# Optimization experiments

Hardware: AMD Instinct MI355X
Metric: run time of the kernel (lower is better)

## Reference

```python
import jax, jax.numpy as jnp
import numpy as np

T, B, K, N, M = 1024, 32, 8, 64, 64
DELTA = 3  # number of passes: DELTA-1 states-only + 1 final with output


def setup_inputs():
    key = jax.random.key(0)
    ks = jax.random.split(key, 7)
    x = jax.random.normal(ks[0], (T, B, K), jnp.float32)
    # stable, a.s.-distinct complex eigenvalues: |lam| in [0.5, 0.99)
    mag = jax.random.uniform(ks[1], (K, N), jnp.float32, 0.5, 0.99)
    phase = jax.random.uniform(ks[2], (K, N), jnp.float32, -np.pi, np.pi)
    lam_re = mag * jnp.cos(phase)
    lam_im = mag * jnp.sin(phase)
    C_re = jax.random.normal(ks[3], (K, N, M), jnp.float32) / np.sqrt(N)
    C_im = jax.random.normal(ks[4], (K, N, M), jnp.float32) / np.sqrt(N)
    D = jax.random.normal(ks[5], (K, M), jnp.float32)
    Do = jax.random.normal(ks[6], (K, M), jnp.float32)
    return {"x": x, "lam_re": lam_re, "lam_im": lam_im,
            "C_re": C_re, "C_im": C_im, "D": D, "Do": Do}


def _compute_Bp(lam):
    # Bʹ[k,j] = exp(-sum_i log(1 - lam_i/lam_j)), diagonal ratio zeroed
    k, n = lam.shape
    ratios = lam[:, :, None] / lam[:, None, :]           # (k, n, n)
    eye = jnp.eye(n, dtype=bool)[None]
    ratios = jnp.where(eye, jnp.zeros((), ratios.dtype), ratios)
    lnBp = -jnp.sum(jnp.log(1.0 - ratios), axis=1)       # (k, n)
    return jnp.exp(lnBp)


def _linear_recurrence(a, bx):
    # s_t = a_t * s_{t-1} + bx_t, computed as a parallel associative scan
    def comb(l, r):
        al, bl = l
        ar, br = r
        return (al * ar, bl * ar + br)
    _, s = jax.lax.associative_scan(comb, (a, bx), axis=0)
    return s


def _states(xc, lam, Bp, alpha):
    # one pass of the complex diagonal SSM; returns states (T, B, K, N)
    Bpx = (xc[..., None] * Bp).reshape(T, B, K * N)       # Bʹ·x
    if alpha is None:
        al = jnp.broadcast_to(lam.reshape(1, 1, K * N), (T, B, K * N))
    else:
        al = (alpha * lam[None, None]).reshape(T, B, K * N)  # α·λ
    # standard=True: shift inputs by one step (prepend zeros, drop last)
    z = jnp.zeros((1, B, K * N), al.dtype)
    al = jnp.concatenate([z, al[:-1]], axis=0)
    Bpx = jnp.concatenate([z, Bpx[:-1]], axis=0)
    return _linear_recurrence(al, Bpx).reshape(T, B, K, N)


def _forward(x, lam_re, lam_im, C_re, C_im, D, Do):
    lam = (lam_re + 1j * lam_im).astype(jnp.complex64)    # (K, N)
    Cp = (C_re + 1j * C_im).astype(jnp.complex64)         # (K, N, M)
    xc = x.astype(jnp.complex64)                          # (T, B, K)
    Bp = _compute_Bp(lam)                                 # (K, N)

    alpha = None
    for _ in range(DELTA - 1):
        s = _states(xc, lam, Bp, alpha)                   # (T, B, K, N)
        ls = lam[None, None] * s                          # λ·sʹ
        alpha = 1.0 / jnp.sqrt(1.0 + ls * jnp.conj(ls))   # recipsq

    s = _states(xc, lam, Bp, alpha)                       # final pass
    Cs = jnp.einsum("tbkn,knm->tbkm", s, Cp)              # Cʹ·sʹ
    Dx = xc[..., None] * D.astype(jnp.complex64)          # D·x
    y = Cs + Dx + Do.astype(jnp.complex64)                # (T, B, K, M)
    return jnp.mean(y, axis=2)                            # average over k


def reference(x, lam_re, lam_im, C_re, C_im, D, Do):
    return _forward(x, lam_re, lam_im, C_re, C_im, D, Do)
```

## Files before the change

### kernel.cpp

```cpp
#include <hip/hip_runtime.h>

#define TT 1024
#define BB 32
#define KKD 8
#define NN 64
#define MM 64
#define BKC (BB*KKD)
#define KN  (KKD*NN)
#define SS 16
#define LL 64

typedef __attribute__((ext_vector_type(8))) _Float16 f16x8;
typedef __attribute__((ext_vector_type(2))) __fp16 fp16x2;
typedef __attribute__((ext_vector_type(4))) float f32x4;

#define SC_DOWN (1.0f/4096.0f)
#define SC_UP   512.0f


static __device__ __forceinline__ float bcast(float v, int lane) {
    return __builtin_bit_cast(float,
        __builtin_amdgcn_readlane(__builtin_bit_cast(int, v), lane));
}

__global__ __launch_bounds__(64) void bp_kernel(const float* __restrict__ lam_re,
                                                const float* __restrict__ lam_im,
                                                float* __restrict__ bp) {
    int k = blockIdx.x;
    int j = threadIdx.x;
    double ljre = (double)lam_re[k*NN+j], ljim = (double)lam_im[k*NN+j];
    double dj = ljre*ljre + ljim*ljim;
    double pre = 1.0, pim = 0.0;
    for (int i = 0; i < NN; ++i) {
        if (i == j) continue;
        double lire = (double)lam_re[k*NN+i], liim = (double)lam_im[k*NN+i];
        double rre = (lire*ljre + liim*ljim)/dj;
        double rim = (liim*ljre - lire*ljim)/dj;
        double zre = 1.0 - rre, zim = -rim;
        double zd = zre*zre + zim*zim;
        double npre = (pre*zre + pim*zim)/zd;
        double npim = (pim*zre - pre*zim)/zd;
        pre = npre; pim = npim;
    }
    bp[(k*NN+j)*2+0] = (float)pre;
    bp[(k*NN+j)*2+1] = (float)pim;
}

__global__ __launch_bounds__(256) void wprep_kernel(const float* __restrict__ C_re,
                                                    const float* __restrict__ C_im,
                                                    unsigned short* __restrict__ Wt) {
    int idx = blockIdx.x*256 + threadIdx.x;
    int m  = idx >> 10;
    int j  = idx & 1023;
    int kn = j >> 1;
    float v = (j & 1) ? -C_im[kn*MM + m] : C_re[kn*MM + m];
    Wt[idx] = __builtin_bit_cast(unsigned short, (_Float16)(v * SC_UP));
}

__global__ __launch_bounds__(1024, 4) void scan_par_kernel(const float* __restrict__ x,
                                                           const float* __restrict__ lam_re,
                                                           const float* __restrict__ lam_im,
                                                           const float* __restrict__ bp,
                                                           unsigned int* __restrict__ abuf,
                                                           int TL) {
    __shared__ float e1[SS][64][2];
    __shared__ float e2[SS][64][2];
    __shared__ float e3[SS][64][2];
    __shared__ float pa2[SS][64];
    __shared__ float pa3[SS][64];

    int bk = blockIdx.x;
    int b = bk >> 3;
    int k = bk & 7;
    int tid = threadIdx.x;
    int q = tid >> 6;
    int n = tid & 63;
    int kn = k*NN + n;
    float lre = lam_re[kn], lim = lam_im[kn];
    float bpre = bp[2*kn+0], bpim = bp[2*kn+1];
    float l2 = lre*lre + lim*lim;

    float p64re = lre, p64im = lim;
    #pragma unroll
    for (int i = 0; i < 6; ++i) {
        float tr = p64re*p64re - p64im*p64im;
        float ti = 2.f*p64re*p64im;
        p64re = tr; p64im = ti;
    }

    const float* xp = x + (size_t)(q*LL)*BKC + b*KKD + k;
    float xs = xp[(size_t)n * BKC];

    float s1re = 0.f, s1im = 0.f;
    #pragma unroll 16
    for (int i = 0; i < LL; ++i) {
        float xv = bcast(xs, i);
        float ure = xv*bpre, uim = xv*bpim;
        float tre = __builtin_fmaf(lre, s1re, __builtin_fmaf(-lim, s1im, ure));
        float tim = __builtin_fmaf(lre, s1im, __builtin_fmaf( lim, s1re, uim));
        s1re = tre; s1im = tim;
    }
    e1[q][n][0] = s1re; e1[q][n][1] = s1im;
    __syncthreads();
    float c1re = 0.f, c1im = 0.f;
    for (int i = 0; i < q; ++i) {
        float tre = __builtin_fmaf(p64re, c1re, __builtin_fmaf(-p64im, c1im, e1[i][n][0]));
        float tim = __builtin_fmaf(p64re, c1im, __builtin_fmaf( p64im, c1re, e1[i][n][1]));
        c1re = tre; c1im = tim;
    }

    s1re = c1re; s1im = c1im;
    float s2re = 0.f, s2im = 0.f, pa = 1.f;
    #pragma unroll 16
    for (int i = 0; i < LL; ++i) {
        float xv = bcast(xs, i);
        float ure = xv*bpre, uim = xv*bpim;
        float mm1 = __builtin_fmaf(l2, __builtin_fmaf(s1re, s1re, s1im*s1im), 1.f);
        float a1 = rsqrtf(mm1);
        float t1re = __builtin_fmaf(lre, s1re, __builtin_fmaf(-lim, s1im, ure));
        float t1im = __builtin_fmaf(lre, s1im, __builtin_fmaf( lim, s1re, uim));
        s1re = t1re; s1im = t1im;
        float cr = a1*lre, ci = a1*lim;
        float t2re = __builtin_fmaf(cr, s2re, __builtin_fmaf(-ci, s2im, ure));
        float t2im = __builtin_fmaf(cr, s2im, __builtin_fmaf( ci, s2re, uim));
        s2re = t2re; s2im = t2im;
        pa *= a1;
    }
    e2[q][n][0] = s2re; e2[q][n][1] = s2im; pa2[q][n] = pa;
    __syncthreads();
    float c2re = 0.f, c2im = 0.f;
    for (int i = 0; i < q; ++i) {
        float pai = pa2[i][n];
        float qre = pai*p64re, qim = pai*p64im;
        float tre = __builtin_fmaf(qre, c2re, __builtin_fmaf(-qim, c2im, e2[i][n][0]));
        float tim = __builtin_fmaf(qre, c2im, __builtin_fmaf( qim, c2re, e2[i][n][1]));
        c2re = tre; c2im = tim;
    }

    s1re = c1re; s1im = c1im;
    s2re = c2re; s2im = c2im;
    float s3re = 0.f, s3im = 0.f, pb = 1.f;
    unsigned int a2pk[LL/2];
    float a2prev = 0.f;
    #pragma unroll
    for (int i = 0; i < LL; ++i) {
        float xv = bcast(xs, i);
        float ure = xv*bpre, uim = xv*bpim;
        float mm1 = __builtin_fmaf(l2, __builtin_fmaf(s1re, s1re, s1im*s1im), 1.f);
        float a1 = rsqrtf(mm1);
        float t1re = __builtin_fmaf(lre, s1re, __builtin_fmaf(-lim, s1im, ure));
        float t1im = __builtin_fmaf(lre, s1im, __builtin_fmaf( lim, s1re, uim));
        s1re = t1re; s1im = t1im;
        float mm2 = __builtin_fmaf(l2, __builtin_fmaf(s2re, s2re, s2im*s2im), 1.f);
        float a2 = rsqrtf(mm2);
        float cr = a1*lre, ci = a1*lim;
        float t2re = __builtin_fmaf(cr, s2re, __builtin_fmaf(-ci, s2im, ure));
        float t2im = __builtin_fmaf(cr, s2im, __builtin_fmaf( ci, s2re, uim));
        s2re = t2re; s2im = t2im;
        float dr = a2*lre, di = a2*lim;
        float t3re = __builtin_fmaf(dr, s3re, __builtin_fmaf(-di, s3im, ure));
        float t3im = __builtin_fmaf(dr, s3im, __builtin_fmaf( di, s3re, uim));
        s3re = t3re; s3im = t3im;
        pb *= a2;
        if (i & 1)
            a2pk[i>>1] = __builtin_bit_cast(unsigned int,
                           __builtin_amdgcn_cvt_pkrtz(a2prev, a2));
        else
            a2prev = a2;
    }
    e3[q][n][0] = s3re; e3[q][n][1] = s3im; pa3[q][n] = pb;
    __syncthreads();
    float c3re = 0.f, c3im = 0.f;
    for (int i = 0; i < q; ++i) {
        float pbi = pa3[i][n];
        float qre = pbi*p64re, qim = pbi*p64im;
        float tre = __builtin_fmaf(qre, c3re, __builtin_fmaf(-qim, c3im, e3[i][n][0]));
        float tim = __builtin_fmaf(qre, c3im, __builtin_fmaf( qim, c3re, e3[i][n][1]));
        c3re = tre; c3im = tim;
    }

    s3re = c3re; s3im = c3im;
    unsigned int* ap = abuf + (size_t)bk*TL*64 + (size_t)(q*LL)*64 + n;
    #pragma unroll
    for (int i = 0; i < LL; ++i) {
        fp16x2 hv = __builtin_amdgcn_cvt_pkrtz(s3re*SC_DOWN, s3im*SC_DOWN);
        ap[(size_t)i * 64] = __builtin_bit_cast(unsigned int, hv);
        float xv = bcast(xs, i);
        float ure = xv*bpre, uim = xv*bpim;
        unsigned int pk = a2pk[i>>1];
        unsigned short h = (i & 1) ? (unsigned short)(pk >> 16)
                                   : (unsigned short)(pk & 0xffffu);
        float a2 = (float)__builtin_bit_cast(_Float16, h);
        float dr = a2*lre, di = a2*lim;
        float t3re = __builtin_fmaf(dr, s3re, __builtin_fmaf(-di, s3im, ure));
        float t3im = __builtin_fmaf(dr, s3im, __builtin_fmaf( di, s3re, uim));
        s3re = t3re; s3im = t3im;
    }
}

__global__ __launch_bounds__(64) void scan_seq_kernel(const float* __restrict__ x,
                                                      const float* __restrict__ lam_re,
                                                      const float* __restrict__ lam_im,
                                                      const float* __restrict__ bp,
                                                      float* __restrict__ state,
                                                      unsigned int* __restrict__ abuf,
                                                      int chunk_start, int chunk_len,
                                                      int TL) {
    int bk = blockIdx.x;
    int b = bk >> 3;
    int k = bk & 7;
    int n = threadIdx.x;
    int kn = k*NN + n;
    float lre = lam_re[kn], lim = lam_im[kn];
    float bpre = bp[2*kn+0], bpim = bp[2*kn+1];
    float l2 = lre*lre + lim*lim;
    int chain = bk*NN + n;

    float s1re,s1im,s2re,s2im,s3re,s3im;
    if (chunk_start == 0) {
        s1re=s1im=s2re=s2im=s3re=s3im=0.f;
    } else {
        const float* st = state + (size_t)chain*6;
        s1re=st[0];s1im=st[1];s2re=st[2];s2im=st[3];s3re=st[4];s3im=st[5];
    }

    const float* xp = x + (size_t)chunk_start*BKC + b*KKD + k;
    unsigned int* ap = abuf + (size_t)bk*TL*64 + n;

    float xs = xp[(size_t)n * BKC];
    for (int t0 = 0; t0 < chunk_len; t0 += 64) {
        float xs_nxt = 0.f;
        if (t0 + 64 < chunk_len) xs_nxt = xp[(size_t)(t0 + 64 + n) * BKC];
        #pragma unroll
        for (int w = 0; w < 4; ++w) {
            float mm_[16], cre[16], cim[16];
            #pragma unroll
            for (int j = 0; j < 16; ++j) {
                float xv = bcast(xs, w*16 + j);
                mm_[j] = __builtin_fmaf(l2, s1re*s1re + s1im*s1im, 1.0f);
                float ure = xv*bpre, uim = xv*bpim;
                float tre = __builtin_fmaf(lre, s1re, __builtin_fmaf(-lim, s1im, ure));
                float tim = __builtin_fmaf(lre, s1im, __builtin_fmaf( lim, s1re, uim));
                s1re=tre; s1im=tim;
            }
            #pragma unroll
            for (int j = 0; j < 16; ++j) {
                float a = rsqrtf(mm_[j]); cre[j] = a*lre; cim[j] = a*lim;
            }
            #pragma unroll
            for (int j = 0; j < 16; ++j) {
                float xv = bcast(xs, w*16 + j);
                mm_[j] = __builtin_fmaf(l2, s2re*s2re + s2im*s2im, 1.0f);
                float ure = xv*bpre, uim = xv*bpim;
                float tre = __builtin_fmaf(cre[j], s2re, __builtin_fmaf(-cim[j], s2im, ure));
                float tim = __builtin_fmaf(cre[j], s2im, __builtin_fmaf( cim[j], s2re, uim));
                s2re=tre; s2im=tim;
            }
            #pragma unroll
            for (int j = 0; j < 16; ++j) {
                float a = rsqrtf(mm_[j]); cre[j] = a*lre; cim[j] = a*lim;
            }
            #pragma unroll
            for (int j = 0; j < 16; ++j) {
                fp16x2 hv = __builtin_amdgcn_cvt_pkrtz(s3re*SC_DOWN, s3im*SC_DOWN);
                ap[(size_t)(t0 + w*16 + j) * 64] = __builtin_bit_cast(unsigned int, hv);
                float xv = bcast(xs, w*16 + j);
                float ure = xv*bpre, uim = xv*bpim;
                float tre = __builtin_fmaf(cre[j], s3re, __builtin_fmaf(-cim[j], s3im, ure));
                float tim = __builtin_fmaf(cre[j], s3im, __builtin_fmaf( cim[j], s3re, uim));
                s3re=tre; s3im=tim;
            }
        }
        xs = xs_nxt;
    }
    float* st = state + (size_t)chain*6;
    st[0]=s1re;st[1]=s1im;st[2]=s2re;st[3]=s2im;st[4]=s3re;st[5]=s3im;
}

__global__ __launch_bounds__(256) void proj_kernel(const unsigned int* __restrict__ A,
                                                   const unsigned short* __restrict__ Wt,
                                                   const float* __restrict__ x,
                                                   const float* __restrict__ D,
                                                   const float* __restrict__ Do,
                                                   float* __restrict__ out,
                                                   int rowOff, int TL) {
    __shared__ uint4 At[2][1024];
    __shared__ uint4 Wb[2][1024];
    int tid = threadIdx.x;
    int w = tid >> 6, l = tid & 63;
    int lg = l >> 4, lr = l & 15;
    int wr = w >> 1, wc = w & 1;
    int bI = blockIdx.x;
    int R0 = bI * 64;

    f32x4 acc[2][2];
    #pragma unroll
    for (int g = 0; g < 2; ++g)
        #pragma unroll
        for (int t = 0; t < 2; ++t) acc[g][t] = (f32x4){0.f,0.f,0.f,0.f};

    uint4 ra[4], rw[4];
    int srow[4], su[4];
    #pragma unroll
    for (int i = 0; i < 4; ++i) {
        int unit = w*256 + i*64 + l;
        srow[i] = unit >> 4;
        su[i]   = unit & 15;
    }

    #pragma unroll
    for (int i = 0; i < 4; ++i) {
        int row = srow[i], u = su[i];
        int b = row & 31, t2 = (bI << 1) + (row >> 5);
        ra[i] = *(const uint4*)((const char*)A + ((((size_t)(b*8 + 0)*TL + t2) << 8) + u*16));
        rw[i] = *(const uint4*)((const char*)Wt + (row*2048 + 0*256 + u*16));
    }
    #pragma unroll
    for (int i = 0; i < 4; ++i) {
        int row = srow[i], u = su[i];
        At[0][row*16 + (u ^ (row & 7))] = ra[i];
        Wb[0][row*16 + (u ^ (row & 7))] = rw[i];
    }
    __syncthreads();

    for (int kc = 0; kc < 8; ++kc) {
        int cur = kc & 1;
        if (kc < 7) {
            int kn = kc + 1;
            #pragma unroll
            for (int i = 0; i < 4; ++i) {
                int row = srow[i], u = su[i];
                int b = row & 31, t2 = (bI << 1) + (row >> 5);
                ra[i] = *(const uint4*)((const char*)A + ((((size_t)(b*8 + kn)*TL + t2) << 8) + u*16));
                rw[i] = *(const uint4*)((const char*)Wt + (row*2048 + kn*256 + u*16));
            }
        }
        #pragma unroll
        for (int ks = 0; ks < 4; ++ks) {
            f16x8 af[2], bf[2];
            #pragma unroll
            for (int g = 0; g < 2; ++g) {
                int row = (wr*2 + g)*16 + lr;
                af[g] = __builtin_bit_cast(f16x8, At[cur][row*16 + ((ks*4 + lg) ^ (row & 7))]);
            }
            #pragma unroll
            for (int t = 0; t < 2; ++t) {
                int m = (wc*2 + t)*16 + lr;
                bf[t] = __builtin_bit_cast(f16x8, Wb[cur][m*16 + ((ks*4 + lg) ^ (m & 7))]);
            }
            #pragma unroll
            for (int g = 0; g < 2; ++g)
                #pragma unroll
                for (int t = 0; t < 2; ++t)
                    acc[g][t] = __builtin_amdgcn_mfma_f32_16x16x32_f16(af[g], bf[t], acc[g][t], 0,0,0);
        }
        if (kc < 7) {
            int nb = (kc + 1) & 1;
            #pragma unroll
            for (int i = 0; i < 4; ++i) {
                int row = srow[i], u = su[i];
                At[nb][row*16 + (u ^ (row & 7))] = ra[i];
                Wb[nb][row*16 + (u ^ (row & 7))] = rw[i];
            }
        }
        __syncthreads();
    }

    #pragma unroll
    for (int g = 0; g < 2; ++g) {
        int rowA = rowOff + R0 + (wr*2 + g)*16 + lr;
        const float* xr = x + (size_t)rowA * KKD;
        float4 x0 = *(const float4*)(xr);
        float4 x1 = *(const float4*)(xr + 4);
        f16x8 a2;
        a2[0] = (lg==0) ? (_Float16)x0.x : ((lg==1) ? (_Float16)1.0f : (_Float16)0.0f);
        a2[1] = (lg==0) ? (_Float16)x0.y : (_Float16)0.0f;
        a2[2] = (lg==0) ? (_Float16)x0.z : (_Float16)0.0f;
        a2[3] = (lg==0) ? (_Float16)x0.w : (_Float16)0.0f;
        a2[4] = (lg==0) ? (_Float16)x1.x : (_Float16)0.0f;
        a2[5] = (lg==0) ? (_Float16)x1.y : (_Float16)0.0f;
        a2[6] = (lg==0) ? (_Float16)x1.z : (_Float16)0.0f;
        a2[7] = (lg==0) ? (_Float16)x1.w : (_Float16)0.0f;
        #pragma unroll
        for (int t = 0; t < 2; ++t) {
            int c = (wc*2 + t)*16 + lr;
            float dob = 0.f;
            #pragma unroll
            for (int i = 0; i < 8; ++i) dob += Do[i*64 + c];
            f16x8 b2;
            b2[0] = (lg==0) ? (_Float16)(D[0*64+c]*0.125f)
                  : ((lg==1) ? (_Float16)(dob*0.125f) : (_Float16)0.0f);
            b2[1] = (lg==0) ? (_Float16)(D[1*64+c]*0.125f) : (_Float16)0.0f;
            b2[2] = (lg==0) ? (_Float16)(D[2*64+c]*0.125f) : (_Float16)0.0f;
            b2[3] = (lg==0) ? (_Float16)(D[3*64+c]*0.125f) : (_Float16)0.0f;
            b2[4] = (lg==0) ? (_Float16)(D[4*64+c]*0.125f) : (_Float16)0.0f;
            b2[5] = (lg==0) ? (_Float16)(D[5*64+c]*0.125f) : (_Float16)0.0f;
            b2[6] = (lg==0) ? (_Float16)(D[6*64+c]*0.125f) : (_Float16)0.0f;
            b2[7] = (lg==0) ? (_Float16)(D[7*64+c]*0.125f) : (_Float16)0.0f;
            acc[g][t] = __builtin_amdgcn_mfma_f32_16x16x32_f16(a2, b2, acc[g][t], 0,0,0);
        }
    }

    #pragma unroll
    for (int g = 0; g < 2; ++g)
        #pragma unroll
        for (int t = 0; t < 2; ++t) {
            int c = (wc*2 + t)*16 + lr;
            #pragma unroll
            for (int reg = 0; reg < 4; ++reg) {
                int row = rowOff + R0 + (wr*2 + g)*16 + lg*4 + reg;
                out[(size_t)row*MM + c] = acc[g][t][reg];
            }
        }
}

extern "C" void kernel_launch(void* const* d_in, const int* in_sizes, int n_in,
                              void* d_out, int out_size, void* d_ws, size_t ws_size,
                              hipStream_t stream) {
    const float* x      = (const float*)d_in[0];
    const float* lam_re = (const float*)d_in[1];
    const float* lam_im = (const float*)d_in[2];
    const float* C_re   = (const float*)d_in[3];
    const float* C_im   = (const float*)d_in[4];
    const float* D      = (const float*)d_in[5];
    const float* Do     = (const float*)d_in[6];
    float* out = (float*)d_out;

    char* ws = (char*)d_ws;
    float*          bpw    = (float*)(ws);
    unsigned short* Wt     = (unsigned short*)(ws + 4096);
    float*          statew = (float*)(ws + 135168);
    unsigned int*   abuf   = (unsigned int*)(ws + 528384);

    bp_kernel<<<KKD, NN, 0, stream>>>(lam_re, lam_im, bpw);
    wprep_kernel<<<256, 256, 0, stream>>>(C_re, C_im, Wt);

    const size_t base = 528384;
    const size_t perT = (size_t)BB*KN*4;

    if (ws_size >= base + (size_t)TT*perT) {
        scan_par_kernel<<<BKC, SS*64, 0, stream>>>(x, lam_re, lam_im, bpw, abuf, TT);
        proj_kernel<<<TT*BB/64, 256, 0, stream>>>(abuf, Wt, x, D, Do, out, 0, TT);
    } else {
        size_t avail = ws_size > base ? ws_size - base : 0;
        int chunkT = (int)(avail / perT) & ~63;
        if (chunkT < 64) chunkT = 64;
        for (int cs = 0; cs < TT; cs += chunkT) {
            int len = (chunkT < TT - cs) ? chunkT : (TT - cs);
            scan_seq_kernel<<<BKC, NN, 0, stream>>>(x, lam_re, lam_im, bpw, statew,
                                                    abuf, cs, len, len);
            proj_kernel<<<len*BB/64, 256, 0, stream>>>(abuf, Wt, x, D, Do, out,
                                                       cs*BB, len);
        }
    }
}
```

Measured before the change: 81.11 us.

## Split scan into 32 segments of 32 steps with half-N per block

The chunked parallel scan now splits each (b,k) problem across two blocks, each handling 32 of the 64 state channels. Each block uses 32 time segments of 32 steps instead of 16 segments of 64, which doubles the grid and halves the serial per-thread recurrence length. The cost is a longer serial carry-combine loop across segments, and x values are now shared with width-32 shuffles instead of readlane. Launch bounds request higher occupancy.

```diff
diff --git a/kernel.cpp b/kernel.cpp
--- a/kernel.cpp
+++ b/kernel.cpp
@@ -7,8 +7,6 @@
 #define MM 64
 #define BKC (BB*KKD)
 #define KN  (KKD*NN)
-#define SS 16
-#define LL 64
 
 typedef __attribute__((ext_vector_type(8))) _Float16 f16x8;
 typedef __attribute__((ext_vector_type(2))) __fp16 fp16x2;
@@ -57,63 +55,68 @@
     Wt[idx] = __builtin_bit_cast(unsigned short, (_Float16)(v * SC_UP));
 }
 
-__global__ __launch_bounds__(1024, 4) void scan_par_kernel(const float* __restrict__ x,
-                                                           const float* __restrict__ lam_re,
-                                                           const float* __restrict__ lam_im,
-                                                           const float* __restrict__ bp,
-                                                           unsigned int* __restrict__ abuf,
-                                                           int TL) {
-    __shared__ float e1[SS][64][2];
-    __shared__ float e2[SS][64][2];
-    __shared__ float e3[SS][64][2];
-    __shared__ float pa2[SS][64];
-    __shared__ float pa3[SS][64];
-
-    int bk = blockIdx.x;
+__global__ __launch_bounds__(1024, 8) void scan_par2_kernel(const float* __restrict__ x,
+                                                            const float* __restrict__ lam_re,
+                                                            const float* __restrict__ lam_im,
+                                                            const float* __restrict__ bp,
+                                                            unsigned int* __restrict__ abuf,
+                                                            int TL) {
+    __shared__ float e1[32][32][2];
+    __shared__ float e2[32][32][2];
+    __shared__ float e3[32][32][2];
+    __shared__ float pa2[32][32];
+    __shared__ float pa3[32][32];
+
+    int blk = blockIdx.x;
+    int bk = blk >> 1;
+    int h  = blk & 1;
     int b = bk >> 3;
     int k = bk & 7;
     int tid = threadIdx.x;
-    int q = tid >> 6;
-    int n = tid & 63;
-    int kn = k*NN + n;
+    int seg = tid >> 5;
+    int nl  = tid & 31;
+    int n   = h*32 + nl;
+    int kn  = k*NN + n;
+    int w    = tid >> 6;
+    int lane = tid & 63;
+
     float lre = lam_re[kn], lim = lam_im[kn];
     float bpre = bp[2*kn+0], bpim = bp[2*kn+1];
     float l2 = lre*lre + lim*lim;
 
-    float p64re = lre, p64im = lim;
-    #pragma unroll
-    for (int i = 0; i < 6; ++i) {
-        float tr = p64re*p64re - p64im*p64im;
-        float ti = 2.f*p64re*p64im;
-        p64re = tr; p64im = ti;
-    }
-
-    const float* xp = x + (size_t)(q*LL)*BKC + b*KKD + k;
-    float xs = xp[(size_t)n * BKC];
+    float p32re = lre, p32im = lim;
+    #pragma unroll
+    for (int i = 0; i < 5; ++i) {
+        float tr = p32re*p32re - p32im*p32im;
+        float ti = 2.f*p32re*p32im;
+        p32re = tr; p32im = ti;
+    }
+
+    float xs = x[(size_t)(w*64 + lane)*BKC + b*KKD + k];
 
     float s1re = 0.f, s1im = 0.f;
-    #pragma unroll 16
-    for (int i = 0; i < LL; ++i) {
-        float xv = bcast(xs, i);
+    #pragma unroll
+    for (int i = 0; i < 32; ++i) {
+        float xv = __shfl(xs, i, 32);
         float ure = xv*bpre, uim = xv*bpim;
         float tre = __builtin_fmaf(lre, s1re, __builtin_fmaf(-lim, s1im, ure));
         float tim = __builtin_fmaf(lre, s1im, __builtin_fmaf( lim, s1re, uim));
         s1re = tre; s1im = tim;
     }
-    e1[q][n][0] = s1re; e1[q][n][1] = s1im;
+    e1[seg][nl][0] = s1re; e1[seg][nl][1] = s1im;
     __syncthreads();
     float c1re = 0.f, c1im = 0.f;
-    for (int i = 0; i < q; ++i) {
-        float tre = __builtin_fmaf(p64re, c1re, __builtin_fmaf(-p64im, c1im, e1[i][n][0]));
-        float tim = __builtin_fmaf(p64re, c1im, __builtin_fmaf( p64im, c1re, e1[i][n][1]));
+    for (int i = 0; i < seg; ++i) {
+        float tre = __builtin_fmaf(p32re, c1re, __builtin_fmaf(-p32im, c1im, e1[i][nl][0]));
+        float tim = __builtin_fmaf(p32re, c1im, __builtin_fmaf( p32im, c1re, e1[i][nl][1]));
         c1re = tre; c1im = tim;
     }
 
     s1re = c1re; s1im = c1im;
     float s2re = 0.f, s2im = 0.f, pa = 1.f;
-    #pragma unroll 16
-    for (int i = 0; i < LL; ++i) {
-        float xv = bcast(xs, i);
+    #pragma unroll
+    for (int i = 0; i < 32; ++i) {
+        float xv = __shfl(xs, i, 32);
         float ure = xv*bpre, uim = xv*bpim;
         float mm1 = __builtin_fmaf(l2, __builtin_fmaf(s1re, s1re, s1im*s1im), 1.f);
         float a1 = rsqrtf(mm1);
@@ -126,25 +129,25 @@
         s2re = t2re; s2im = t2im;
         pa *= a1;
     }
-    e2[q][n][0] = s2re; e2[q][n][1] = s2im; pa2[q][n] = pa;
+    e2[seg][nl][0] = s2re; e2[seg][nl][1] = s2im; pa2[seg][nl] = pa;
     __syncthreads();
     float c2re = 0.f, c2im = 0.f;
-    for (int i = 0; i < q; ++i) {
-        float pai = pa2[i][n];
-        float qre = pai*p64re, qim = pai*p64im;
-        float tre = __builtin_fmaf(qre, c2re, __builtin_fmaf(-qim, c2im, e2[i][n][0]));
-        float tim = __builtin_fmaf(qre, c2im, __builtin_fmaf( qim, c2re, e2[i][n][1]));
+    for (int i = 0; i < seg; ++i) {
+        float pai = pa2[i][nl];
+        float qre = pai*p32re, qim = pai*p32im;
+        float tre = __builtin_fmaf(qre, c2re, __builtin_fmaf(-qim, c2im, e2[i][nl][0]));
+        float tim = __builtin_fmaf(qre, c2im, __builtin_fmaf( qim, c2re, e2[i][nl][1]));
         c2re = tre; c2im = tim;
     }
 
     s1re = c1re; s1im = c1im;
     s2re = c2re; s2im = c2im;
     float s3re = 0.f, s3im = 0.f, pb = 1.f;
-    unsigned int a2pk[LL/2];
+    unsigned int a2pk[16];
     float a2prev = 0.f;
     #pragma unroll
-    for (int i = 0; i < LL; ++i) {
-        float xv = bcast(xs, i);
+    for (int i = 0; i < 32; ++i) {
+        float xv = __shfl(xs, i, 32);
         float ure = xv*bpre, uim = xv*bpim;
         float mm1 = __builtin_fmaf(l2, __builtin_fmaf(s1re, s1re, s1im*s1im), 1.f);
         float a1 = rsqrtf(mm1);
@@ -168,29 +171,29 @@
         else
             a2prev = a2;
     }
-    e3[q][n][0] = s3re; e3[q][n][1] = s3im; pa3[q][n] = pb;
+    e3[seg][nl][0] = s3re; e3[seg][nl][1] = s3im; pa3[seg][nl] = pb;
     __syncthreads();
     float c3re = 0.f, c3im = 0.f;
-    for (int i = 0; i < q; ++i) {
-        float pbi = pa3[i][n];
-        float qre = pbi*p64re, qim = pbi*p64im;
-        float tre = __builtin_fmaf(qre, c3re, __builtin_fmaf(-qim, c3im, e3[i][n][0]));
-        float tim = __builtin_fmaf(qre, c3im, __builtin_fmaf( qim, c3re, e3[i][n][1]));
+    for (int i = 0; i < seg; ++i) {
+        float pbi = pa3[i][nl];
+        float qre = pbi*p32re, qim = pbi*p32im;
+        float tre = __builtin_fmaf(qre, c3re, __builtin_fmaf(-qim, c3im, e3[i][nl][0]));
+        float tim = __builtin_fmaf(qre, c3im, __builtin_fmaf( qim, c3re, e3[i][nl][1]));
         c3re = tre; c3im = tim;
     }
 
     s3re = c3re; s3im = c3im;
-    unsigned int* ap = abuf + (size_t)bk*TL*64 + (size_t)(q*LL)*64 + n;
-    #pragma unroll
-    for (int i = 0; i < LL; ++i) {
+    unsigned int* ap = abuf + ((size_t)bk*TL + seg*32)*64 + n;
+    #pragma unroll
+    for (int i = 0; i < 32; ++i) {
         fp16x2 hv = __builtin_amdgcn_cvt_pkrtz(s3re*SC_DOWN, s3im*SC_DOWN);
         ap[(size_t)i * 64] = __builtin_bit_cast(unsigned int, hv);
-        float xv = bcast(xs, i);
+        float xv = __shfl(xs, i, 32);
         float ure = xv*bpre, uim = xv*bpim;
         unsigned int pk = a2pk[i>>1];
-        unsigned short h = (i & 1) ? (unsigned short)(pk >> 16)
-                                   : (unsigned short)(pk & 0xffffu);
-        float a2 = (float)__builtin_bit_cast(_Float16, h);
+        unsigned short hh = (i & 1) ? (unsigned short)(pk >> 16)
+                                    : (unsigned short)(pk & 0xffffu);
+        float a2 = (float)__builtin_bit_cast(_Float16, hh);
         float dr = a2*lre, di = a2*lim;
         float t3re = __builtin_fmaf(dr, s3re, __builtin_fmaf(-di, s3im, ure));
         float t3im = __builtin_fmaf(dr, s3im, __builtin_fmaf( di, s3re, uim));
@@ -439,7 +442,7 @@
     const size_t perT = (size_t)BB*KN*4;
 
     if (ws_size >= base + (size_t)TT*perT) {
-        scan_par_kernel<<<BKC, SS*64, 0, stream>>>(x, lam_re, lam_im, bpw, abuf, TT);
+        scan_par2_kernel<<<BKC*2, 1024, 0, stream>>>(x, lam_re, lam_im, bpw, abuf, TT);
         proj_kernel<<<TT*BB/64, 256, 0, stream>>>(abuf, Wt, x, D, Do, out, 0, TT);
     } else {
         size_t avail = ws_size > base ? ws_size - base : 0;
```

Result: slower. 87.49 us (+7.9%).
